# Optimization experiments

Hardware: AMD Instinct MI355X
Metric: run time of the kernel (lower is better)

Reference implementation:

```python
import jax, jax.numpy as jnp
import numpy as np

D_MODEL = 1024
NUM_HEADS = 16
HEAD_DIM = D_MODEL // NUM_HEADS  # 64
ROPE_THETA = 10000.0
SEQ_LEN = 4096
BATCH = 1


def apply_rope(x, positions, theta=ROPE_THETA):
    # x: [b, h, s, d], positions: [s]
    d = x.shape[-1]
    inv_freq = theta ** (-jnp.arange(0, d, 2, dtype=jnp.float32) / d)  # [d/2]
    angles = positions.astype(jnp.float32)[:, None] * inv_freq[None, :]  # [s, d/2]
    cos = jnp.cos(angles)  # [s, d/2]
    sin = jnp.sin(angles)
    x1 = x[..., 0::2]  # [b, h, s, d/2]
    x2 = x[..., 1::2]
    r1 = x1 * cos - x2 * sin
    r2 = x1 * sin + x2 * cos
    # interleave back to [..., d]
    out = jnp.stack([r1, r2], axis=-1).reshape(x.shape)
    return out.astype(x.dtype)


def setup_inputs() -> dict:
    key = jax.random.key(0)
    k_x, k_qkv, k_o = jax.random.split(key, 3)
    scale_in = 1.0 / np.sqrt(D_MODEL)
    return {
        "x": jax.random.normal(k_x, (BATCH, SEQ_LEN, D_MODEL), dtype=jnp.float32),
        "token_positions": jnp.arange(SEQ_LEN, dtype=jnp.int64 if jax.config.jax_enable_x64 else jnp.int32),
        "w_qkv": jax.random.normal(k_qkv, (3 * D_MODEL, D_MODEL), dtype=jnp.float32) * scale_in,
        "w_o": jax.random.normal(k_o, (D_MODEL, D_MODEL), dtype=jnp.float32) * scale_in,
    }


def reference(x, token_positions, w_qkv, w_o):
    b, s, _ = x.shape
    # QKV projection (Linear without bias, weight [out, in])
    x_qkv = jnp.einsum('bsd,ed->bse', x, w_qkv)  # [b, s, 3*d_model]
    # rearrange 'b s (three heads kv) -> three b heads s kv'
    x_qkv = x_qkv.reshape(b, s, 3, NUM_HEADS, HEAD_DIM)
    x_qkv = jnp.transpose(x_qkv, (2, 0, 3, 1, 4))  # [3, b, h, s, d]
    q, k, v = x_qkv[0], x_qkv[1], x_qkv[2]
    q = apply_rope(q, token_positions)
    k = apply_rope(k, token_positions)
    # scaled dot-product attention with causal mask
    scores = jnp.einsum('bhnd,bhmd->bhnm', q, k) / jnp.sqrt(jnp.float32(HEAD_DIM))
    causal = jnp.tril(jnp.ones((s, s), dtype=bool))  # [s, s]
    scores = jnp.where(causal[None, None], scores, jnp.float32(-jnp.inf))
    weights = jax.nn.softmax(scores, axis=-1)
    attn = jnp.einsum('bhnm,bhmd->bhnd', weights, v)  # [b, h, s, d]
    attn = jnp.transpose(attn, (0, 2, 1, 3)).reshape(b, s, NUM_HEADS * HEAD_DIM)
    return jnp.einsum('bsd,ed->bse', attn, w_o)
```

## Files before the change

kernel.cpp:

```cpp
#include <hip/hip_runtime.h>

#define SEQ 4096
#define DMODEL 1024
#define HEADS 16
#define HD 64
#define NQKV 3072

typedef __attribute__((ext_vector_type(8))) __bf16 bf16x8;
typedef __attribute__((ext_vector_type(4))) __bf16 bf16x4;
typedef __attribute__((ext_vector_type(8))) short short8;
typedef __attribute__((ext_vector_type(4))) float f32x4;

__device__ __forceinline__ unsigned short f2bf(float f) {
    unsigned u = __builtin_bit_cast(unsigned, f);
    return (unsigned short)((u + 0x7fffu + ((u >> 16) & 1u)) >> 16);
}
__device__ __forceinline__ float bf2f(unsigned short h) {
    return __builtin_bit_cast(float, (unsigned)h << 16);
}

__device__ __forceinline__ void gload16(const void* g, void* l) {
    __builtin_amdgcn_global_load_lds(
        (const __attribute__((address_space(1))) unsigned int*)g,
        (__attribute__((address_space(3))) unsigned int*)l, 16, 0, 0);
}

__global__ void f2bf_all(const float* __restrict__ x, const float* __restrict__ wqkv,
                         const float* __restrict__ wo, unsigned short* __restrict__ dst) {
    const int N0 = SEQ * DMODEL / 4;
    const int N1 = N0 + NQKV * DMODEL / 4;
    const int NT = N1 + DMODEL * DMODEL / 4;
    int i = blockIdx.x * 256 + threadIdx.x;
    int stride = gridDim.x * 256;
    for (; i < NT; i += stride) {
        const float4* src;
        if (i < N0)      src = reinterpret_cast<const float4*>(x) + i;
        else if (i < N1) src = reinterpret_cast<const float4*>(wqkv) + (i - N0);
        else             src = reinterpret_cast<const float4*>(wo) + (i - N1);
        float4 f = *src;
        ushort4 o;
        o.x = f2bf(f.x); o.y = f2bf(f.y); o.z = f2bf(f.z); o.w = f2bf(f.w);
        reinterpret_cast<ushort4*>(dst)[i] = o;
    }
}

template <int EPI>
__global__ __launch_bounds__(256) void gemm_bt(const unsigned short* __restrict__ A,
                                               const unsigned short* __restrict__ B,
                                               float* __restrict__ outF,
                                               unsigned short* __restrict__ outB,
                                               int M, int N, int K) {
    alignas(16) __shared__ unsigned short a_lds[2][128 * 32];
    alignas(16) __shared__ unsigned short b_lds[2][128 * 32];
    const int tid = threadIdx.x;
    const int wave = tid >> 6, lane = tid & 63;
    const int l16 = lane & 15, g = lane >> 4;
    const int wr = wave >> 1, wc = wave & 1;
    const int bm = blockIdx.x, bn = blockIdx.y;

    const int lrow = lane >> 2;
    const int lcol = (lane & 3) * 8;

    const unsigned short* Ag = A + (size_t)(bm * 128 + lrow) * K + lcol;
    const unsigned short* Bg = B + (size_t)(bn * 128 + lrow) * K + lcol;

    f32x4 acc[4][4] = {};
    const int NS = K / 32;

    auto STAGE = [&](int b, int ks) {
#pragma unroll
        for (int j = 0; j < 2; ++j) {
            int chunk = wave * 2 + j;
            gload16(Ag + (size_t)(chunk * 16) * K + ks * 32, a_lds[b] + chunk * 512);
            gload16(Bg + (size_t)(chunk * 16) * K + ks * 32, b_lds[b] + chunk * 512);
        }
    };

    STAGE(0, 0);

    for (int ks = 0; ks < NS; ++ks) {
        const int cur = ks & 1;
        asm volatile("s_waitcnt vmcnt(0)" ::: "memory");
        __builtin_amdgcn_s_barrier();
        if (ks + 1 < NS) STAGE(cur ^ 1, ks + 1);

        bf16x8 af[4], bfr[4];
#pragma unroll
        for (int m = 0; m < 4; ++m)
            af[m] = *reinterpret_cast<const bf16x8*>(a_lds[cur] + (wr * 64 + m * 16 + l16) * 32 + g * 8);
#pragma unroll
        for (int n = 0; n < 4; ++n)
            bfr[n] = *reinterpret_cast<const bf16x8*>(b_lds[cur] + (wc * 64 + n * 16 + l16) * 32 + g * 8);
        __builtin_amdgcn_s_setprio(1);
#pragma unroll
        for (int m = 0; m < 4; ++m)
#pragma unroll
            for (int n = 0; n < 4; ++n)
                acc[m][n] = __builtin_amdgcn_mfma_f32_16x16x32_bf16(af[m], bfr[n], acc[m][n], 0, 0, 0);
        __builtin_amdgcn_s_setprio(0);
    }

#pragma unroll
    for (int m = 0; m < 4; ++m)
#pragma unroll
        for (int n = 0; n < 4; ++n)
#pragma unroll
            for (int r = 0; r < 4; ++r) {
                int row = bm * 128 + wr * 64 + m * 16 + g * 4 + r;
                int col = bn * 128 + wc * 64 + n * 16 + l16;
                float v = acc[m][n][r];
                if (EPI == 0) {
                    int part = col >> 10;
                    int hd = col & 1023;
                    int h = hd >> 6, d = hd & 63;
                    outB[(size_t)((part * HEADS + h) * SEQ + row) * HD + d] = f2bf(v);
                } else {
                    outF[(size_t)row * N + col] = v;
                }
            }
}

__global__ __launch_bounds__(256) void rope_kernel(unsigned short* qkv, const int* __restrict__ pos) {
    int idx = blockIdx.x * 256 + threadIdx.x;
    int chunk = idx & 7;
    int row = idx >> 3;
    int s = row & (SEQ - 1);
    int ph = row >> 12;
    float p = (float)pos[s];
    float scale = (ph < HEADS) ? 0.125f * 1.4426950408889634f : 1.0f;
    unsigned short* base = qkv + ((size_t)ph * SEQ + s) * HD + chunk * 8;
    short8 v = *reinterpret_cast<short8*>(base);
    short8 o;
    const float k = -13.287712379549449f / 32.0f;
#pragma unroll
    for (int j = 0; j < 4; ++j) {
        int i = chunk * 4 + j;
        float ang = p * exp2f((float)i * k);
        float sn, cs;
        sincosf(ang, &sn, &cs);
        float x1 = bf2f((unsigned short)v[2 * j]);
        float x2 = bf2f((unsigned short)v[2 * j + 1]);
        o[2 * j]     = (short)f2bf((x1 * cs - x2 * sn) * scale);
        o[2 * j + 1] = (short)f2bf((x1 * sn + x2 * cs) * scale);
    }
    *reinterpret_cast<short8*>(base) = o;
}

__global__ __launch_bounds__(256) void transpose_v(const unsigned short* __restrict__ qkv,
                                                   unsigned short* __restrict__ vt) {
    const int st = blockIdx.x;
    const int h = blockIdx.y;
    __shared__ unsigned short tile[64][72];
    const unsigned short* Vg = qkv + (size_t)((2 * HEADS + h) * SEQ) * HD;
    const int tid = threadIdx.x;
#pragma unroll
    for (int j = 0; j < 2; ++j) {
        int b = (tid + j * 256) * 8;
        int row = b >> 6;
        int col = b & 63;
        short8 v = *reinterpret_cast<const short8*>(Vg + (size_t)(st * 64 + row) * HD + col);
#pragma unroll
        for (int i = 0; i < 8; ++i) tile[row][col + i] = (unsigned short)v[i];
    }
    __syncthreads();
#pragma unroll
    for (int j = 0; j < 2; ++j) {
        int b = (tid + j * 256) * 8;
        int d = b >> 6;
        int sc = b & 63;
        short8 o;
#pragma unroll
        for (int i = 0; i < 8; ++i) o[i] = (short)tile[sc + i][d];
        *reinterpret_cast<short8*>(vt + (size_t)(h * HD + d) * SEQ + st * 64 + sc) = o;
    }
}

__global__ __launch_bounds__(512) void attn_kernel(const unsigned short* __restrict__ qkv,
                                                   const unsigned short* __restrict__ vt,
                                                   unsigned short* __restrict__ attnout,
                                                   int* __restrict__ qcnt,
                                                   unsigned short* __restrict__ pO,
                                                   float* __restrict__ lmf) {
    const int xcd = blockIdx.x & 7;
    const int tid = threadIdx.x;
    const int wave = tid >> 6, lane = tid & 63;
    const int l16 = lane & 15, g = lane >> 4;

    alignas(16) __shared__ unsigned short k_lds[2][128 * 64];
    alignas(16) __shared__ unsigned short v_lds[2][2][64 * 64];
    alignas(16) __shared__ unsigned short p_lds[8][16 * 64];
    __shared__ int slot_sh;

    char* pwave = (char*)p_lds + wave * 2048;
    const int rsw = (l16 & 7) << 4;

    for (;;) {
        if (tid == 0) slot_sh = atomicAdd(&qcnt[xcd], 1);
        __syncthreads();
        const int t = slot_sh;
        __syncthreads();
        if (t >= 108) break;

        int qtile, hloc, khalf, k0, k1;
        bool isSplit;
        if (t < 88) {
            qtile = 31 - (t >> 2);
            hloc = (t >> 1) & 1;
            khalf = t & 1;
            int T = qtile + 1, H = (T + 1) >> 1;
            k0 = khalf ? H : 0;
            k1 = khalf ? T : H;
            isSplit = true;
        } else {
            int rem = t - 88;
            qtile = 9 - (rem >> 1);
            hloc = rem & 1;
            khalf = 0;
            k0 = 0; k1 = qtile + 1;
            isSplit = false;
        }
        const int h = xcd * 2 + hloc;

        const unsigned short* Qg = qkv + (size_t)((0 * HEADS + h) * SEQ) * HD;
        const unsigned short* Kg = qkv + (size_t)((1 * HEADS + h) * SEQ) * HD;
        const unsigned short* VTg = vt + (size_t)h * HD * SEQ;

        const int qbase = qtile * 128 + wave * 16;
        bf16x8 qf[2];
        qf[0] = *reinterpret_cast<const bf16x8*>(Qg + (size_t)(qbase + l16) * HD + g * 8);
        qf[1] = *reinterpret_cast<const bf16x8*>(Qg + (size_t)(qbase + l16) * HD + 32 + g * 8);

        bf16x8 ones;
#pragma unroll
        for (int j2 = 0; j2 < 8; ++j2) ones[j2] = (__bf16)1.0f;

        f32x4 o_acc[4] = {};
        f32x4 l_acc = {};
        float m_r = -1e30f;

        auto STAGE = [&](int b, int kt) {
#pragma unroll
            for (int i = 0; i < 2; ++i) {
                int base = wave * 2048 + i * 1024;
                int byte = base + lane * 16;
                int krow = byte >> 7;
                int kc8 = ((byte >> 4) & 7) ^ (krow & 7);
                gload16(Kg + (size_t)(kt * 128 + krow) * HD + kc8 * 8, (char*)k_lds[b] + base);
                int fr = byte >> 7;
                int h64 = fr >> 6, vd = fr & 63;
                int vc8 = ((byte >> 4) & 7) ^ (vd & 7);
                gload16(VTg + (size_t)vd * SEQ + kt * 128 + h64 * 64 + vc8 * 8,
                        (char*)v_lds[b] + base);
            }
        };

        STAGE(0, k0);

        for (int kt = k0; kt < k1; ++kt) {
            const int cur = (kt - k0) & 1;
            asm volatile("s_waitcnt vmcnt(0)" ::: "memory");
            __builtin_amdgcn_s_barrier();
            if (kt + 1 < k1) STAGE(cur ^ 1, kt + 1);

            const bool doB = (kt * 128 + 64) <= (qbase + 15);

            f32x4 s[8] = {};
            __builtin_amdgcn_s_setprio(1);
#pragma unroll
            for (int nt = 0; nt < 4; ++nt) {
                int row = nt * 16 + l16;
#pragma unroll
                for (int kk = 0; kk < 2; ++kk) {
                    bf16x8 kf = *reinterpret_cast<const bf16x8*>(
                        (char*)k_lds[cur] + row * 128 + (((kk * 4 + g) << 4) ^ rsw));
                    s[nt] = __builtin_amdgcn_mfma_f32_16x16x32_bf16(kf, qf[kk], s[nt], 0, 0, 0);
                }
            }
            if (doB) {
#pragma unroll
                for (int nt = 0; nt < 4; ++nt) {
                    int row = 64 + nt * 16 + l16;
#pragma unroll
                    for (int kk = 0; kk < 2; ++kk) {
                        bf16x8 kf = *reinterpret_cast<const bf16x8*>(
                            (char*)k_lds[cur] + row * 128 + (((kk * 4 + g) << 4) ^ rsw));
                        s[4 + nt] = __builtin_amdgcn_mfma_f32_16x16x32_bf16(kf, qf[kk], s[4 + nt], 0, 0, 0);
                    }
                }
            }
            __builtin_amdgcn_s_setprio(0);

            if (kt * 128 + 127 > qbase) {
                int qrow = qbase + l16;
#pragma unroll
                for (int nt = 0; nt < 4; ++nt)
#pragma unroll
                    for (int r = 0; r < 4; ++r) {
                        int kv = kt * 128 + nt * 16 + g * 4 + r;
                        if (kv > qrow) s[nt][r] = -1e30f;
                        if (kv + 64 > qrow) s[4 + nt][r] = -1e30f;
                    }
            }

            f32x4 m4;
#pragma unroll
            for (int r = 0; r < 4; ++r) {
                float a = fmaxf(fmaxf(s[0][r], s[1][r]), fmaxf(s[2][r], s[3][r]));
                float b = fmaxf(fmaxf(s[4][r], s[5][r]), fmaxf(s[6][r], s[7][r]));
                m4[r] = fmaxf(a, b);
            }
            float mx = fmaxf(fmaxf(m4[0], m4[1]), fmaxf(m4[2], m4[3]));
            mx = fmaxf(mx, __shfl_xor(mx, 16));
            mx = fmaxf(mx, __shfl_xor(mx, 32));

            if (__any(mx > m_r + 8.0f)) {
                float mnew = fmaxf(m_r, mx);
                float alpha = __builtin_amdgcn_exp2f(m_r - mnew);
                m_r = mnew;
#pragma unroll
                for (int dt = 0; dt < 4; ++dt)
#pragma unroll
                    for (int r = 0; r < 4; ++r) o_acc[dt][r] *= alpha;
                l_acc[0] *= alpha;
            }

#pragma unroll
            for (int i = 0; i < 8; ++i)
#pragma unroll
                for (int r = 0; r < 4; ++r) s[i][r] = __builtin_amdgcn_exp2f(s[i][r] - m_r);

            __builtin_amdgcn_s_setprio(1);
#pragma unroll
            for (int h64 = 0; h64 < 2; ++h64) {
                if (h64 && !doB) break;
#pragma unroll
                for (int nt = 0; nt < 4; ++nt) {
                    bf16x4 pb;
#pragma unroll
                    for (int r = 0; r < 4; ++r) pb[r] = (__bf16)s[h64 * 4 + nt][r];
                    *reinterpret_cast<bf16x4*>(pwave + l16 * 128 + ((nt * 32 + g * 8) ^ rsw)) = pb;
                }
                bf16x8 pfrag[2];
#pragma unroll
                for (int kk = 0; kk < 2; ++kk)
                    pfrag[kk] = *reinterpret_cast<const bf16x8*>(
                        pwave + l16 * 128 + (((kk * 4 + g) << 4) ^ rsw));

#pragma unroll
                for (int dt = 0; dt < 4; ++dt) {
                    int row = dt * 16 + l16;
#pragma unroll
                    for (int kk = 0; kk < 2; ++kk) {
                        bf16x8 vf = *reinterpret_cast<const bf16x8*>(
                            (char*)v_lds[cur][h64] + row * 128 + (((kk * 4 + g) << 4) ^ rsw));
                        o_acc[dt] = __builtin_amdgcn_mfma_f32_16x16x32_bf16(vf, pfrag[kk], o_acc[dt], 0, 0, 0);
                    }
                }
                l_acc = __builtin_amdgcn_mfma_f32_16x16x32_bf16(ones, pfrag[0], l_acc, 0, 0, 0);
                l_acc = __builtin_amdgcn_mfma_f32_16x16x32_bf16(ones, pfrag[1], l_acc, 0, 0, 0);
            }
            __builtin_amdgcn_s_setprio(0);
        }

        const int ql = wave * 16 + l16;
        if (isSplit) {
            int sidx = (h * 22 + (qtile - 10)) * 2 + khalf;
            unsigned short* Op = pO + (size_t)sidx * 8192;
#pragma unroll
            for (int dt = 0; dt < 4; ++dt) {
                ushort4 ov;
                ov.x = f2bf(o_acc[dt][0]);
                ov.y = f2bf(o_acc[dt][1]);
                ov.z = f2bf(o_acc[dt][2]);
                ov.w = f2bf(o_acc[dt][3]);
                *reinterpret_cast<ushort4*>(Op + ql * 64 + dt * 16 + g * 4) = ov;
            }
            if (g == 0) {
                lmf[sidx * 256 + ql] = l_acc[0];
                lmf[sidx * 256 + 128 + ql] = m_r;
            }
        } else {
            float inv = 1.0f / l_acc[0];
            int q = qtile * 128 + ql;
#pragma unroll
            for (int dt = 0; dt < 4; ++dt) {
                ushort4 ov;
                ov.x = f2bf(o_acc[dt][0] * inv);
                ov.y = f2bf(o_acc[dt][1] * inv);
                ov.z = f2bf(o_acc[dt][2] * inv);
                ov.w = f2bf(o_acc[dt][3] * inv);
                *reinterpret_cast<ushort4*>(attnout + (size_t)q * DMODEL + h * HD + dt * 16 + g * 4) = ov;
            }
        }
    }
}

__global__ __launch_bounds__(256) void merge_kernel(const unsigned short* __restrict__ pO,
                                                    const float* __restrict__ lmf,
                                                    unsigned short* __restrict__ attnout) {
    int idx = blockIdx.x * 256 + threadIdx.x;
    if (idx >= 16 * 22 * 1024) return;
    int h = idx / (22 * 1024);
    int r = idx % (22 * 1024);
    int qt = r >> 10;
    int rr = r & 1023;
    int q = rr >> 3, d8 = rr & 7;

    int s0 = (h * 22 + qt) * 2;
    float l0 = lmf[s0 * 256 + q],       m0 = lmf[s0 * 256 + 128 + q];
    float l1 = lmf[(s0 + 1) * 256 + q], m1 = lmf[(s0 + 1) * 256 + 128 + q];
    float m = fmaxf(m0, m1);
    float a0 = __builtin_amdgcn_exp2f(m0 - m), a1 = __builtin_amdgcn_exp2f(m1 - m);
    float L = l0 * a0 + l1 * a1;
    float c0 = a0 / L, c1 = a1 / L;

    const unsigned short* O0 = pO + (size_t)s0 * 8192 + q * 64 + d8 * 8;
    const unsigned short* O1 = O0 + 8192;
    short8 v0 = *reinterpret_cast<const short8*>(O0);
    short8 v1 = *reinterpret_cast<const short8*>(O1);
    short8 o;
#pragma unroll
    for (int j = 0; j < 8; ++j) {
        float val = bf2f((unsigned short)v0[j]) * c0 + bf2f((unsigned short)v1[j]) * c1;
        o[j] = (short)f2bf(val);
    }
    int qtile = qt + 10;
    *reinterpret_cast<short8*>(attnout + (size_t)(qtile * 128 + q) * DMODEL + h * HD + d8 * 8) = o;
}

extern "C" void kernel_launch(void* const* d_in, const int* in_sizes, int n_in,
                              void* d_out, int out_size, void* d_ws, size_t ws_size,
                              hipStream_t stream) {
    const float* x = (const float*)d_in[0];
    const int* pos = (const int*)d_in[1];
    const float* wqkv = (const float*)d_in[2];
    const float* wo = (const float*)d_in[3];
    float* out = (float*)d_out;

    unsigned short* xb = (unsigned short*)d_ws;
    unsigned short* wqkvb = xb + (size_t)SEQ * DMODEL;
    unsigned short* wob = wqkvb + (size_t)NQKV * DMODEL;
    unsigned short* qkvp = wob + (size_t)DMODEL * DMODEL;
    unsigned short* vt = qkvp + (size_t)3 * HEADS * SEQ * HD;
    unsigned short* attnb = vt + (size_t)HEADS * HD * SEQ;

    char* sbase = (char*)d_ws;
    int* qcnt = (int*)sbase;
    float* lmf = (float*)(sbase + 256);
    unsigned short* pO = (unsigned short*)(sbase + 256 + (1 << 20));

    f2bf_all<<<2048, 256, 0, stream>>>(x, wqkv, wo, xb);

    dim3 g1(SEQ / 128, NQKV / 128);
    gemm_bt<0><<<g1, 256, 0, stream>>>(xb, wqkvb, nullptr, qkvp, SEQ, NQKV, DMODEL);

    rope_kernel<<<(2 * HEADS * SEQ * 8) / 256, 256, 0, stream>>>(qkvp, pos);
    transpose_v<<<dim3(SEQ / 64, HEADS), 256, 0, stream>>>(qkvp, vt);

    hipMemsetAsync(qcnt, 0, 64, stream);
    attn_kernel<<<512, 512, 0, stream>>>(qkvp, vt, attnb, qcnt, pO, lmf);
    merge_kernel<<<(16 * 22 * 1024 + 255) / 256, 256, 0, stream>>>(pO, lmf, attnb);

    dim3 g2(SEQ / 128, DMODEL / 128);
    gemm_bt<1><<<g2, 256, 0, stream>>>(attnb, wob, out, nullptr, SEQ, DMODEL, DMODEL);
}
```

Before: 166.2 us.

## Replace atomic persistent scheduler with static one-block-per-task grid

Removes the persistent-block atomic work queue in the attention kernel, and the memset that reset its counter. Each block now reads its task from a constant table interleaving split halves of large q-tiles with whole small q-tiles. The split threshold moves from q-tile 10 to 16, so fewer tiles are split and the merge kernel shrinks. The aim is to drop the atomic and memset overhead and rebalance the causal work, at the risk of a worse tail since blocks are no longer scheduled dynamically.

```diff
diff --git a/kernel.cpp b/kernel.cpp
--- a/kernel.cpp
+++ b/kernel.cpp
@@ -24,6 +24,20 @@
         (const __attribute__((address_space(1))) unsigned int*)g,
         (__attribute__((address_space(3))) unsigned int*)l, 16, 0, 0);
 }
+
+#define TS(qt, kh) (0x40 | ((kh) << 5) | (qt))
+__device__ __constant__ unsigned char TASKS[48] = {
+    TS(31,0), TS(31,1), TS(30,0), 15,
+    TS(30,1), TS(29,0), TS(29,1), TS(28,0), 14,
+    TS(28,1), TS(27,0), TS(27,1), TS(26,0), 13,
+    TS(26,1), TS(25,0), TS(25,1), TS(24,0), 12,
+    TS(24,1), TS(23,0), TS(23,1), TS(22,0), 11,
+    TS(22,1), TS(21,0), TS(21,1), TS(20,0), 10,
+    TS(20,1), TS(19,0), TS(19,1), TS(18,0), 9,
+    TS(18,1), TS(17,0), TS(17,1), TS(16,0), 8,
+    TS(16,1), 7,
+    6, 5, 4, 3, 2, 1, 0
+};
 
 __global__ void f2bf_all(const float* __restrict__ x, const float* __restrict__ wqkv,
                          const float* __restrict__ wo, unsigned short* __restrict__ dst) {
@@ -178,10 +192,21 @@
 __global__ __launch_bounds__(512) void attn_kernel(const unsigned short* __restrict__ qkv,
                                                    const unsigned short* __restrict__ vt,
                                                    unsigned short* __restrict__ attnout,
-                                                   int* __restrict__ qcnt,
                                                    unsigned short* __restrict__ pO,
                                                    float* __restrict__ lmf) {
-    const int xcd = blockIdx.x & 7;
+    const int bid = blockIdx.x;
+    const int xcd = bid & 7;
+    const int slot = bid >> 3;
+    const int hloc = slot & 1;
+    const unsigned char e = TASKS[slot >> 1];
+    const int qtile = e & 31;
+    const int khalf = (e >> 5) & 1;
+    const bool isSplit = (e >> 6) != 0;
+    const int T = qtile + 1, Hh = (T + 1) >> 1;
+    const int k0 = isSplit ? (khalf ? Hh : 0) : 0;
+    const int k1 = isSplit ? (khalf ? T : Hh) : T;
+    const int h = xcd * 2 + hloc;
+
     const int tid = threadIdx.x;
     const int wave = tid >> 6, lane = tid & 63;
     const int l16 = lane & 15, g = lane >> 4;
@@ -189,208 +214,179 @@
     alignas(16) __shared__ unsigned short k_lds[2][128 * 64];
     alignas(16) __shared__ unsigned short v_lds[2][2][64 * 64];
     alignas(16) __shared__ unsigned short p_lds[8][16 * 64];
-    __shared__ int slot_sh;
+
+    const unsigned short* Qg = qkv + (size_t)((0 * HEADS + h) * SEQ) * HD;
+    const unsigned short* Kg = qkv + (size_t)((1 * HEADS + h) * SEQ) * HD;
+    const unsigned short* VTg = vt + (size_t)h * HD * SEQ;
+
+    const int qbase = qtile * 128 + wave * 16;
+    bf16x8 qf[2];
+    qf[0] = *reinterpret_cast<const bf16x8*>(Qg + (size_t)(qbase + l16) * HD + g * 8);
+    qf[1] = *reinterpret_cast<const bf16x8*>(Qg + (size_t)(qbase + l16) * HD + 32 + g * 8);
+
+    bf16x8 ones;
+#pragma unroll
+    for (int j2 = 0; j2 < 8; ++j2) ones[j2] = (__bf16)1.0f;
+
+    f32x4 o_acc[4] = {};
+    f32x4 l_acc = {};
+    float m_r = -1e30f;
 
     char* pwave = (char*)p_lds + wave * 2048;
     const int rsw = (l16 & 7) << 4;
 
-    for (;;) {
-        if (tid == 0) slot_sh = atomicAdd(&qcnt[xcd], 1);
-        __syncthreads();
-        const int t = slot_sh;
-        __syncthreads();
-        if (t >= 108) break;
-
-        int qtile, hloc, khalf, k0, k1;
-        bool isSplit;
-        if (t < 88) {
-            qtile = 31 - (t >> 2);
-            hloc = (t >> 1) & 1;
-            khalf = t & 1;
-            int T = qtile + 1, H = (T + 1) >> 1;
-            k0 = khalf ? H : 0;
-            k1 = khalf ? T : H;
-            isSplit = true;
-        } else {
-            int rem = t - 88;
-            qtile = 9 - (rem >> 1);
-            hloc = rem & 1;
-            khalf = 0;
-            k0 = 0; k1 = qtile + 1;
-            isSplit = false;
-        }
-        const int h = xcd * 2 + hloc;
-
-        const unsigned short* Qg = qkv + (size_t)((0 * HEADS + h) * SEQ) * HD;
-        const unsigned short* Kg = qkv + (size_t)((1 * HEADS + h) * SEQ) * HD;
-        const unsigned short* VTg = vt + (size_t)h * HD * SEQ;
-
-        const int qbase = qtile * 128 + wave * 16;
-        bf16x8 qf[2];
-        qf[0] = *reinterpret_cast<const bf16x8*>(Qg + (size_t)(qbase + l16) * HD + g * 8);
-        qf[1] = *reinterpret_cast<const bf16x8*>(Qg + (size_t)(qbase + l16) * HD + 32 + g * 8);
-
-        bf16x8 ones;
-#pragma unroll
-        for (int j2 = 0; j2 < 8; ++j2) ones[j2] = (__bf16)1.0f;
-
-        f32x4 o_acc[4] = {};
-        f32x4 l_acc = {};
-        float m_r = -1e30f;
-
-        auto STAGE = [&](int b, int kt) {
-#pragma unroll
-            for (int i = 0; i < 2; ++i) {
-                int base = wave * 2048 + i * 1024;
-                int byte = base + lane * 16;
-                int krow = byte >> 7;
-                int kc8 = ((byte >> 4) & 7) ^ (krow & 7);
-                gload16(Kg + (size_t)(kt * 128 + krow) * HD + kc8 * 8, (char*)k_lds[b] + base);
-                int fr = byte >> 7;
-                int h64 = fr >> 6, vd = fr & 63;
-                int vc8 = ((byte >> 4) & 7) ^ (vd & 7);
-                gload16(VTg + (size_t)vd * SEQ + kt * 128 + h64 * 64 + vc8 * 8,
-                        (char*)v_lds[b] + base);
+    auto STAGE = [&](int b, int kt) {
+#pragma unroll
+        for (int i = 0; i < 2; ++i) {
+            int base = wave * 2048 + i * 1024;
+            int byte = base + lane * 16;
+            int krow = byte >> 7;
+            int kc8 = ((byte >> 4) & 7) ^ (krow & 7);
+            gload16(Kg + (size_t)(kt * 128 + krow) * HD + kc8 * 8, (char*)k_lds[b] + base);
+            int fr = byte >> 7;
+            int h64 = fr >> 6, vd = fr & 63;
+            int vc8 = ((byte >> 4) & 7) ^ (vd & 7);
+            gload16(VTg + (size_t)vd * SEQ + kt * 128 + h64 * 64 + vc8 * 8,
+                    (char*)v_lds[b] + base);
+        }
+    };
+
+    STAGE(0, k0);
+
+    for (int kt = k0; kt < k1; ++kt) {
+        const int cur = (kt - k0) & 1;
+        asm volatile("s_waitcnt vmcnt(0)" ::: "memory");
+        __builtin_amdgcn_s_barrier();
+        if (kt + 1 < k1) STAGE(cur ^ 1, kt + 1);
+
+        const bool doB = (kt * 128 + 64) <= (qbase + 15);
+
+        f32x4 s[8] = {};
+        __builtin_amdgcn_s_setprio(1);
+#pragma unroll
+        for (int nt = 0; nt < 4; ++nt) {
+            int row = nt * 16 + l16;
+#pragma unroll
+            for (int kk = 0; kk < 2; ++kk) {
+                bf16x8 kf = *reinterpret_cast<const bf16x8*>(
+                    (char*)k_lds[cur] + row * 128 + (((kk * 4 + g) << 4) ^ rsw));
+                s[nt] = __builtin_amdgcn_mfma_f32_16x16x32_bf16(kf, qf[kk], s[nt], 0, 0, 0);
             }
-        };
-
-        STAGE(0, k0);
-
-        for (int kt = k0; kt < k1; ++kt) {
-            const int cur = (kt - k0) & 1;
-            asm volatile("s_waitcnt vmcnt(0)" ::: "memory");
-            __builtin_amdgcn_s_barrier();
-            if (kt + 1 < k1) STAGE(cur ^ 1, kt + 1);
-
-            const bool doB = (kt * 128 + 64) <= (qbase + 15);
-
-            f32x4 s[8] = {};
-            __builtin_amdgcn_s_setprio(1);
+        }
+        if (doB) {
 #pragma unroll
             for (int nt = 0; nt < 4; ++nt) {
-                int row = nt * 16 + l16;
+                int row = 64 + nt * 16 + l16;
 #pragma unroll
                 for (int kk = 0; kk < 2; ++kk) {
                     bf16x8 kf = *reinterpret_cast<const bf16x8*>(
                         (char*)k_lds[cur] + row * 128 + (((kk * 4 + g) << 4) ^ rsw));
-                    s[nt] = __builtin_amdgcn_mfma_f32_16x16x32_bf16(kf, qf[kk], s[nt], 0, 0, 0);
+                    s[4 + nt] = __builtin_amdgcn_mfma_f32_16x16x32_bf16(kf, qf[kk], s[4 + nt], 0, 0, 0);
                 }
             }
-            if (doB) {
-#pragma unroll
-                for (int nt = 0; nt < 4; ++nt) {
-                    int row = 64 + nt * 16 + l16;
-#pragma unroll
-                    for (int kk = 0; kk < 2; ++kk) {
-                        bf16x8 kf = *reinterpret_cast<const bf16x8*>(
-                            (char*)k_lds[cur] + row * 128 + (((kk * 4 + g) << 4) ^ rsw));
-                        s[4 + nt] = __builtin_amdgcn_mfma_f32_16x16x32_bf16(kf, qf[kk], s[4 + nt], 0, 0, 0);
-                    }
+        }
+        __builtin_amdgcn_s_setprio(0);
+
+        if (kt * 128 + 127 > qbase) {
+            int qrow = qbase + l16;
+#pragma unroll
+            for (int nt = 0; nt < 4; ++nt)
+#pragma unroll
+                for (int r = 0; r < 4; ++r) {
+                    int kv = kt * 128 + nt * 16 + g * 4 + r;
+                    if (kv > qrow) s[nt][r] = -1e30f;
+                    if (kv + 64 > qrow) s[4 + nt][r] = -1e30f;
+                }
+        }
+
+        f32x4 m4;
+#pragma unroll
+        for (int r = 0; r < 4; ++r) {
+            float a = fmaxf(fmaxf(s[0][r], s[1][r]), fmaxf(s[2][r], s[3][r]));
+            float b = fmaxf(fmaxf(s[4][r], s[5][r]), fmaxf(s[6][r], s[7][r]));
+            m4[r] = fmaxf(a, b);
+        }
+        float mx = fmaxf(fmaxf(m4[0], m4[1]), fmaxf(m4[2], m4[3]));
+        mx = fmaxf(mx, __shfl_xor(mx, 16));
+        mx = fmaxf(mx, __shfl_xor(mx, 32));
+
+        if (__any(mx > m_r + 8.0f)) {
+            float mnew = fmaxf(m_r, mx);
+            float alpha = __builtin_amdgcn_exp2f(m_r - mnew);
+            m_r = mnew;
+#pragma unroll
+            for (int dt = 0; dt < 4; ++dt)
+#pragma unroll
+                for (int r = 0; r < 4; ++r) o_acc[dt][r] *= alpha;
+            l_acc[0] *= alpha;
+        }
+
+#pragma unroll
+        for (int i = 0; i < 8; ++i)
+#pragma unroll
+            for (int r = 0; r < 4; ++r) s[i][r] = __builtin_amdgcn_exp2f(s[i][r] - m_r);
+
+        __builtin_amdgcn_s_setprio(1);
+#pragma unroll
+        for (int h64 = 0; h64 < 2; ++h64) {
+            if (h64 && !doB) break;
+#pragma unroll
+            for (int nt = 0; nt < 4; ++nt) {
+                bf16x4 pb;
+#pragma unroll
+                for (int r = 0; r < 4; ++r) pb[r] = (__bf16)s[h64 * 4 + nt][r];
+                *reinterpret_cast<bf16x4*>(pwave + l16 * 128 + ((nt * 32 + g * 8) ^ rsw)) = pb;
+            }
+            bf16x8 pfrag[2];
+#pragma unroll
+            for (int kk = 0; kk < 2; ++kk)
+                pfrag[kk] = *reinterpret_cast<const bf16x8*>(
+                    pwave + l16 * 128 + (((kk * 4 + g) << 4) ^ rsw));
+
+#pragma unroll
+            for (int dt = 0; dt < 4; ++dt) {
+                int row = dt * 16 + l16;
+#pragma unroll
+                for (int kk = 0; kk < 2; ++kk) {
+                    bf16x8 vf = *reinterpret_cast<const bf16x8*>(
+                        (char*)v_lds[cur][h64] + row * 128 + (((kk * 4 + g) << 4) ^ rsw));
+                    o_acc[dt] = __builtin_amdgcn_mfma_f32_16x16x32_bf16(vf, pfrag[kk], o_acc[dt], 0, 0, 0);
                 }
             }
-            __builtin_amdgcn_s_setprio(0);
-
-            if (kt * 128 + 127 > qbase) {
-                int qrow = qbase + l16;
-#pragma unroll
-                for (int nt = 0; nt < 4; ++nt)
-#pragma unroll
-                    for (int r = 0; r < 4; ++r) {
-                        int kv = kt * 128 + nt * 16 + g * 4 + r;
-                        if (kv > qrow) s[nt][r] = -1e30f;
-                        if (kv + 64 > qrow) s[4 + nt][r] = -1e30f;
-                    }
-            }
-
-            f32x4 m4;
-#pragma unroll
-            for (int r = 0; r < 4; ++r) {
-                float a = fmaxf(fmaxf(s[0][r], s[1][r]), fmaxf(s[2][r], s[3][r]));
-                float b = fmaxf(fmaxf(s[4][r], s[5][r]), fmaxf(s[6][r], s[7][r]));
-                m4[r] = fmaxf(a, b);
-            }
-            float mx = fmaxf(fmaxf(m4[0], m4[1]), fmaxf(m4[2], m4[3]));
-            mx = fmaxf(mx, __shfl_xor(mx, 16));
-            mx = fmaxf(mx, __shfl_xor(mx, 32));
-
-            if (__any(mx > m_r + 8.0f)) {
-                float mnew = fmaxf(m_r, mx);
-                float alpha = __builtin_amdgcn_exp2f(m_r - mnew);
-                m_r = mnew;
-#pragma unroll
-                for (int dt = 0; dt < 4; ++dt)
-#pragma unroll
-                    for (int r = 0; r < 4; ++r) o_acc[dt][r] *= alpha;
-                l_acc[0] *= alpha;
-            }
-
-#pragma unroll
-            for (int i = 0; i < 8; ++i)
-#pragma unroll
-                for (int r = 0; r < 4; ++r) s[i][r] = __builtin_amdgcn_exp2f(s[i][r] - m_r);
-
-            __builtin_amdgcn_s_setprio(1);
-#pragma unroll
-            for (int h64 = 0; h64 < 2; ++h64) {
-                if (h64 && !doB) break;
-#pragma unroll
-                for (int nt = 0; nt < 4; ++nt) {
-                    bf16x4 pb;
-#pragma unroll
-                    for (int r = 0; r < 4; ++r) pb[r] = (__bf16)s[h64 * 4 + nt][r];
-                    *reinterpret_cast<bf16x4*>(pwave + l16 * 128 + ((nt * 32 + g * 8) ^ rsw)) = pb;
-                }
-                bf16x8 pfrag[2];
-#pragma unroll
-                for (int kk = 0; kk < 2; ++kk)
-                    pfrag[kk] = *reinterpret_cast<const bf16x8*>(
-                        pwave + l16 * 128 + (((kk * 4 + g) << 4) ^ rsw));
-
-#pragma unroll
-                for (int dt = 0; dt < 4; ++dt) {
-                    int row = dt * 16 + l16;
-#pragma unroll
-                    for (int kk = 0; kk < 2; ++kk) {
-                        bf16x8 vf = *reinterpret_cast<const bf16x8*>(
-                            (char*)v_lds[cur][h64] + row * 128 + (((kk * 4 + g) << 4) ^ rsw));
-                        o_acc[dt] = __builtin_amdgcn_mfma_f32_16x16x32_bf16(vf, pfrag[kk], o_acc[dt], 0, 0, 0);
-                    }
-                }
-                l_acc = __builtin_amdgcn_mfma_f32_16x16x32_bf16(ones, pfrag[0], l_acc, 0, 0, 0);
-                l_acc = __builtin_amdgcn_mfma_f32_16x16x32_bf16(ones, pfrag[1], l_acc, 0, 0, 0);
-            }
-            __builtin_amdgcn_s_setprio(0);
-        }
-
-        const int ql = wave * 16 + l16;
-        if (isSplit) {
-            int sidx = (h * 22 + (qtile - 10)) * 2 + khalf;
-            unsigned short* Op = pO + (size_t)sidx * 8192;
-#pragma unroll
-            for (int dt = 0; dt < 4; ++dt) {
-                ushort4 ov;
-                ov.x = f2bf(o_acc[dt][0]);
-                ov.y = f2bf(o_acc[dt][1]);
-                ov.z = f2bf(o_acc[dt][2]);
-                ov.w = f2bf(o_acc[dt][3]);
-                *reinterpret_cast<ushort4*>(Op + ql * 64 + dt * 16 + g * 4) = ov;
-            }
-            if (g == 0) {
-                lmf[sidx * 256 + ql] = l_acc[0];
-                lmf[sidx * 256 + 128 + ql] = m_r;
-            }
-        } else {
-            float inv = 1.0f / l_acc[0];
-            int q = qtile * 128 + ql;
-#pragma unroll
-            for (int dt = 0; dt < 4; ++dt) {
-                ushort4 ov;
-                ov.x = f2bf(o_acc[dt][0] * inv);
-                ov.y = f2bf(o_acc[dt][1] * inv);
-                ov.z = f2bf(o_acc[dt][2] * inv);
-                ov.w = f2bf(o_acc[dt][3] * inv);
-                *reinterpret_cast<ushort4*>(attnout + (size_t)q * DMODEL + h * HD + dt * 16 + g * 4) = ov;
-            }
+            l_acc = __builtin_amdgcn_mfma_f32_16x16x32_bf16(ones, pfrag[0], l_acc, 0, 0, 0);
+            l_acc = __builtin_amdgcn_mfma_f32_16x16x32_bf16(ones, pfrag[1], l_acc, 0, 0, 0);
+        }
+        __builtin_amdgcn_s_setprio(0);
+    }
+
+    const int ql = wave * 16 + l16;
+    if (isSplit) {
+        int sidx = (h * 16 + (qtile - 16)) * 2 + khalf;
+        unsigned short* Op = pO + (size_t)sidx * 8192;
+#pragma unroll
+        for (int dt = 0; dt < 4; ++dt) {
+            ushort4 ov;
+            ov.x = f2bf(o_acc[dt][0]);
+            ov.y = f2bf(o_acc[dt][1]);
+            ov.z = f2bf(o_acc[dt][2]);
+            ov.w = f2bf(o_acc[dt][3]);
+            *reinterpret_cast<ushort4*>(Op + ql * 64 + dt * 16 + g * 4) = ov;
+        }
+        if (g == 0) {
+            lmf[sidx * 256 + ql] = l_acc[0];
+            lmf[sidx * 256 + 128 + ql] = m_r;
+        }
+    } else {
+        float inv = 1.0f / l_acc[0];
+        int q = qtile * 128 + ql;
+#pragma unroll
+        for (int dt = 0; dt < 4; ++dt) {
+            ushort4 ov;
+            ov.x = f2bf(o_acc[dt][0] * inv);
+            ov.y = f2bf(o_acc[dt][1] * inv);
+            ov.z = f2bf(o_acc[dt][2] * inv);
+            ov.w = f2bf(o_acc[dt][3] * inv);
+            *reinterpret_cast<ushort4*>(attnout + (size_t)q * DMODEL + h * HD + dt * 16 + g * 4) = ov;
         }
     }
 }
@@ -399,14 +395,14 @@
                                                     const float* __restrict__ lmf,
                                                     unsigned short* __restrict__ attnout) {
     int idx = blockIdx.x * 256 + threadIdx.x;
-    if (idx >= 16 * 22 * 1024) return;
-    int h = idx / (22 * 1024);
-    int r = idx % (22 * 1024);
+    if (idx >= 16 * 16 * 1024) return;
+    int h = idx / (16 * 1024);
+    int r = idx % (16 * 1024);
     int qt = r >> 10;
     int rr = r & 1023;
     int q = rr >> 3, d8 = rr & 7;
 
-    int s0 = (h * 22 + qt) * 2;
+    int s0 = (h * 16 + qt) * 2;
     float l0 = lmf[s0 * 256 + q],       m0 = lmf[s0 * 256 + 128 + q];
     float l1 = lmf[(s0 + 1) * 256 + q], m1 = lmf[(s0 + 1) * 256 + 128 + q];
     float m = fmaxf(m0, m1);
@@ -424,7 +420,7 @@
         float val = bf2f((unsigned short)v0[j]) * c0 + bf2f((unsigned short)v1[j]) * c1;
         o[j] = (short)f2bf(val);
     }
-    int qtile = qt + 10;
+    int qtile = qt + 16;
     *reinterpret_cast<short8*>(attnout + (size_t)(qtile * 128 + q) * DMODEL + h * HD + d8 * 8) = o;
 }
 
@@ -445,9 +441,8 @@
     unsigned short* attnb = vt + (size_t)HEADS * HD * SEQ;
 
     char* sbase = (char*)d_ws;
-    int* qcnt = (int*)sbase;
-    float* lmf = (float*)(sbase + 256);
-    unsigned short* pO = (unsigned short*)(sbase + 256 + (1 << 20));
+    float* lmf = (float*)sbase;
+    unsigned short* pO = (unsigned short*)(sbase + (1 << 20));
 
     f2bf_all<<<2048, 256, 0, stream>>>(x, wqkv, wo, xb);
 
@@ -457,9 +452,8 @@
     rope_kernel<<<(2 * HEADS * SEQ * 8) / 256, 256, 0, stream>>>(qkvp, pos);
     transpose_v<<<dim3(SEQ / 64, HEADS), 256, 0, stream>>>(qkvp, vt);
 
-    hipMemsetAsync(qcnt, 0, 64, stream);
-    attn_kernel<<<512, 512, 0, stream>>>(qkvp, vt, attnb, qcnt, pO, lmf);
-    merge_kernel<<<(16 * 22 * 1024 + 255) / 256, 256, 0, stream>>>(pO, lmf, attnb);
+    attn_kernel<<<768, 512, 0, stream>>>(qkvp, vt, attnb, pO, lmf);
+    merge_kernel<<<(16 * 16 * 1024 + 255) / 256, 256, 0, stream>>>(pO, lmf, attnb);
 
     dim3 g2(SEQ / 128, DMODEL / 128);
     gemm_bt<1><<<g2, 256, 0, stream>>>(attnb, wob, out, nullptr, SEQ, DMODEL, DMODEL);
```

Result: faster. 148.6 us (-10.6%).
